# Optimization experiments

Hardware: AMD Instinct MI355X
Metric: run time of the kernel (lower is better)

Reference implementation:

```python
import jax, jax.numpy as jnp
import numpy as np
import math

EPS = 1e-5

def make_coords(H, W):
    # Faithful port of generate_coordinates (batch-independent; channels 8,9 stay zero).
    cy = H / 2.0 - 0.5
    cx = W / 2.0 - 0.5
    gx, gy = np.meshgrid(np.arange(H, dtype=np.float32), np.arange(W, dtype=np.float32), indexing='ij')
    two_pi = 2.0 * math.pi
    theta = np.arctan2(gy - cx, gx - cy) % two_pi
    theta = np.round(10000.0 * theta) / 10000.0
    coords = np.zeros((H, W, 18), dtype=np.float32)
    adds = [(1, 1), (1, 0), (1, -1), (0, 1), None, (0, -1), (-1, 1), (-1, 0), (-1, -1)]
    for k, add in enumerate(adds):
        if add is None:
            continue  # center tap offset left at zero (as in source)
        n = k if k < 4 else k - 1
        a = theta + n * (two_pi / 8.0)
        coords[:, :, 2 * k] = np.cos(a) + add[0]
        coords[:, :, 2 * k + 1] = np.sin(a) + add[1]
    return jnp.asarray(coords)

def bilinear_sample(x, py, px):
    # x: [B,C,H,W]; py/px: [H,W] sample coords; zero outside boundaries (torchvision semantics).
    H, W = x.shape[2], x.shape[3]
    y0f = jnp.floor(py); x0f = jnp.floor(px)
    wy1 = py - y0f; wy0 = 1.0 - wy1
    wx1 = px - x0f; wx0 = 1.0 - wx1
    def gather(yf, xf):
        valid = ((yf >= 0) & (yf < H) & (xf >= 0) & (xf < W)).astype(x.dtype)
        yi = jnp.clip(yf, 0, H - 1).astype(jnp.int32)
        xi = jnp.clip(xf, 0, W - 1).astype(jnp.int32)
        return x[:, :, yi, xi] * valid  # [B,C,H,W]
    return (gather(y0f, x0f) * (wy0 * wx0) + gather(y0f, x0f + 1) * (wy0 * wx1)
            + gather(y0f + 1, x0f) * (wy1 * wx0) + gather(y0f + 1, x0f + 1) * (wy1 * wx1))

def deform_conv(x, coords, weight, pad=1):
    # x: [B,Cin,H,W]; coords: [H,W,18] with (dy,dx) pairs per 3x3 tap; weight: [Cout,Cin,3,3]; no bias.
    B, C, H, W = x.shape
    ys = jnp.arange(H, dtype=x.dtype)[:, None]
    xs = jnp.arange(W, dtype=x.dtype)[None, :]
    out = jnp.zeros((B, weight.shape[0], H, W), x.dtype)
    for k in range(9):  # fixed 3x3 taps
        kh, kw = k // 3, k % 3
        py = ys - pad + kh + coords[..., 2 * k]
        px = xs - pad + kw + coords[..., 2 * k + 1]
        samp = bilinear_sample(x, py, px)
        out = out + jnp.einsum('bchw,oc->bohw', samp, weight[:, :, kh, kw])
    return out

def bn_relu(x, gamma, beta):
    # BatchNorm2d in training mode (batch statistics, biased variance) + ReLU.
    mu = x.mean(axis=(0, 2, 3), keepdims=True)
    var = ((x - mu) ** 2).mean(axis=(0, 2, 3), keepdims=True)
    xn = (x - mu) * jax.lax.rsqrt(var + EPS)
    return jax.nn.relu(xn * gamma[None, :, None, None] + beta[None, :, None, None])

def maxpool2(x):
    B, C, H, W = x.shape
    return x.reshape(B, C, H // 2, 2, W // 2, 2).max(axis=(3, 5))

def setup_inputs() -> dict:
    key = jax.random.key(0)
    ks = jax.random.split(key, 16)
    B = 1024
    def conv_w(k, co, ci):
        return jax.random.normal(k, (co, ci, 3, 3), jnp.float32) * (1.0 / np.sqrt(ci * 9))
    inp = {
        'x': jax.random.normal(ks[0], (B, 1, 32, 32), jnp.float32),
        'w11': conv_w(ks[1], 32, 1),  'g11': jnp.ones(32),  'b11': jnp.zeros(32),
        'w12': conv_w(ks[2], 32, 32), 'g12': jnp.ones(32),  'b12': jnp.zeros(32),
        'w21': conv_w(ks[3], 64, 32), 'g21': jnp.ones(64),  'b21': jnp.zeros(64),
        'w22': conv_w(ks[4], 64, 64), 'g22': jnp.ones(64),  'b22': jnp.zeros(64),
        'w31': conv_w(ks[5], 128, 64),  'g31': jnp.ones(128), 'b31': jnp.zeros(128),
        'w32': conv_w(ks[6], 128, 128), 'g32': jnp.ones(128), 'b32': jnp.zeros(128),
        'fcw': jax.random.normal(ks[7], (10, 128), jnp.float32) * (1.0 / np.sqrt(128)),
        'fcb': jnp.zeros(10),
        'c32': make_coords(32, 32),
        'c16': make_coords(16, 16),
        'c8': make_coords(8, 8),
    }
    return inp

def reference(x, w11, g11, b11, w12, g12, b12, w21, g21, b21, w22, g22, b22,
              w31, g31, b31, w32, g32, b32, fcw, fcb, c32, c16, c8):
    x = bn_relu(deform_conv(x, c32, w11), g11, b11)
    x = bn_relu(deform_conv(x, c32, w12), g12, b12)
    x = maxpool2(x)                      # [B,32,16,16]
    x = bn_relu(deform_conv(x, c16, w21), g21, b21)
    x = bn_relu(deform_conv(x, c16, w22), g22, b22)
    x = maxpool2(x)                      # [B,64,8,8]
    x = bn_relu(deform_conv(x, c8, w31), g31, b31)
    x = bn_relu(deform_conv(x, c8, w32), g32, b32)
    x = x.mean(axis=(2, 3))              # AvgPool2d(8) over full 8x8 -> [B,128]
    return x @ fcw.T + fcb               # [B,10]
```

## Files before the change

### kernel.cpp

```cpp
#include <hip/hip_runtime.h>
#include <math.h>


#define BATCH 1024
typedef unsigned short u16;
typedef unsigned int uint;
typedef __attribute__((ext_vector_type(8))) short short8;
typedef __attribute__((ext_vector_type(4))) float f32x4;
typedef __attribute__((ext_vector_type(2))) float f32x2;

__device__ __forceinline__ float b2f(u16 v) {
    return __uint_as_float(((uint)v) << 16);
}
__device__ __forceinline__ float4 b2f4(ushort4 v) {
    return make_float4(b2f(v.x), b2f(v.y), b2f(v.z), b2f(v.w));
}
__device__ __forceinline__ u16 f2b(float f) {
    uint u = __float_as_uint(f);
    return (u16)((u + 0x7FFFu + ((u >> 16) & 1u)) >> 16);
}
__device__ __forceinline__ float ldf(const void* p, long long i, int isbf) {
    return isbf ? b2f(((const u16*)p)[i]) : ((const float*)p)[i];
}
__device__ __forceinline__ f32x2 upk(uint u) {
    f32x2 r;
    r.x = __uint_as_float(u << 16);
    r.y = __uint_as_float(u & 0xFFFF0000u);
    return r;
}

struct Ptrs { const void* p[24]; int sz[24]; };

__global__ __launch_bounds__(256) void probe_dtype(Ptrs P, int* __restrict__ flags)
{
    int t = blockIdx.x;
    bool ones = (t == 2 || t == 5 || t == 8 || t == 11 || t == 14 || t == 17);
    bool inh  = (t == 3 || t == 6 || t == 9 || t == 12 || t == 15 || t == 18 || t == 20);
    if (inh) return;
    const u16* q = (const u16*)P.p[t];
    if (ones) {
        if (threadIdx.x == 0) {
            uint w0 = *(const uint*)q;
            flags[t] = (w0 == 0x3F803F80u) ? 1 : 0;
        }
        return;
    }
    int n = P.sz[t]; if (n > 4096) n = 4096;
    __shared__ int cnt;
    if (threadIdx.x == 0) cnt = 0;
    __syncthreads();
    int local = 0;
    for (int i = threadIdx.x; i < n; i += 256) {
        uint e = (q[i] >> 7) & 0xFFu;
        if (!(e == 0u || (e >= 100u && e <= 140u))) local++;
    }
    atomicAdd(&cnt, local);
    __syncthreads();
    if (threadIdx.x == 0) flags[t] = (cnt * 8 > n) ? 0 : 1;
}

__global__ void fixup_flags(int* __restrict__ flags)
{
    if (threadIdx.x == 0) {
        flags[3] = flags[2];  flags[6] = flags[5];  flags[9] = flags[8];
        flags[12] = flags[11]; flags[15] = flags[14]; flags[18] = flags[17];
        flags[20] = flags[19];
    }
}

__device__ void table_body(const void* coords, int H, int W,
                           int* tIdx, float* tW, int fcd, int i)
{
    int HW = H * W;
    if (i >= HW * 9) return;
    int p = i / 9, k = i % 9;
    int h = p / W, w = p % W;
    int kh = k / 3, kw = k % 3;
    float py = (float)(h - 1 + kh) + ldf(coords, p * 18 + 2 * k, fcd);
    float px = (float)(w - 1 + kw) + ldf(coords, p * 18 + 2 * k + 1, fcd);
    float y0f = floorf(py), x0f = floorf(px);
    float wy1 = py - y0f, wy0 = 1.0f - wy1;
    float wx1 = px - x0f, wx0 = 1.0f - wx1;
    int y0 = (int)y0f, x0 = (int)x0f;
#pragma unroll
    for (int j = 0; j < 4; ++j) {
        int dy = j >> 1, dx = j & 1;
        int yy = y0 + dy, xx = x0 + dx;
        bool valid = (yy >= 0) && (yy < H) && (xx >= 0) && (xx < W);
        int yc = min(max(yy, 0), H - 1);
        int xc = min(max(xx, 0), W - 1);
        tIdx[i * 4 + j] = yc * W + xc;
        tW[i * 4 + j] = valid ? (dy ? wy1 : wy0) * (dx ? wx1 : wx0) : 0.0f;
    }
}

__global__ __launch_bounds__(256) void build_tables(
    const void* c32, const void* c16, const void* c8,
    int* tI32, float* tW32, int* tI16, float* tW16, int* tI8, float* tW8,
    const int* __restrict__ flags)
{
    int b = blockIdx.x, t = threadIdx.x;
    if (b < 36)      table_body(c32, 32, 32, tI32, tW32, flags[21], b * 256 + t);
    else if (b < 45) table_body(c16, 16, 16, tI16, tW16, flags[22], (b - 36) * 256 + t);
    else             table_body(c8, 8, 8, tI8, tW8, flags[23], (b - 45) * 256 + t);
}

__global__ __launch_bounds__(256) void transpose_in(
    const void* __restrict__ x, u16* __restrict__ X0, const int* __restrict__ flags)
{
    int fx = flags[0];
    int p = blockIdx.x;
    int t = threadIdx.x;
    ushort4 v;
    v.x = f2b(ldf(x, (long long)(4 * t + 0) * 1024 + p, fx));
    v.y = f2b(ldf(x, (long long)(4 * t + 1) * 1024 + p, fx));
    v.z = f2b(ldf(x, (long long)(4 * t + 2) * 1024 + p, fx));
    v.w = f2b(ldf(x, (long long)(4 * t + 3) * 1024 + p, fx));
    ((ushort4*)(X0 + (size_t)p * BATCH))[t] = v;
}

__device__ void wb_body(const void* W, u16* Wb, int Cout, int Cin, int fw, int i)
{
    int c8 = i & 7;
    int r = i >> 3;
    int m = r % Cout;
    int r2 = r / Cout;
    int noct = Cin >> 3;
    int oc = r2 % noct;
    int k = r2 / noct;
    int c = oc * 8 + c8;
    Wb[i] = f2b(ldf(W, (long long)m * Cin * 9 + c * 9 + k, fw));
}

__global__ __launch_bounds__(256) void prep_all(
    const void* w11, const void* w12, const void* w21, const void* w22,
    const void* w31, const void* w32,
    float* w11p, u16* wb12, u16* wb21, u16* wb22, u16* wb31, u16* wb32,
    const int* __restrict__ flags)
{
    int i = blockIdx.x * 256 + threadIdx.x;
    if (i < 288) {
        int o = i / 9, k = i % 9;
        w11p[k * 32 + o] = ldf(w11, i, flags[1]);
    } else if (i < 9504)   wb_body(w12, wb12, 32, 32, flags[4], i - 288);
    else if (i < 27936)    wb_body(w21, wb21, 64, 32, flags[7], i - 9504);
    else if (i < 64800)    wb_body(w22, wb22, 64, 64, flags[10], i - 27936);
    else if (i < 138528)   wb_body(w31, wb31, 128, 64, flags[13], i - 64800);
    else if (i < 285984)   wb_body(w32, wb32, 128, 128, flags[16], i - 138528);
}

__global__ __launch_bounds__(256) void conv_l11(
    const u16* __restrict__ X0, const float* __restrict__ W2,
    u16* __restrict__ Y, const int* __restrict__ tIdx, const float* __restrict__ tW)
{
    const int id = blockIdx.x;
    const int p = id >> 1;
    const int oBase = (id & 1) * 16;
    const int b4 = threadIdx.x;
    const ushort4* Xu = (const ushort4*)X0;

    float4 acc[16];
#pragma unroll
    for (int o = 0; o < 16; ++o) acc[o] = make_float4(0.f, 0.f, 0.f, 0.f);

#pragma unroll
    for (int k = 0; k < 9; ++k) {
        float4 s = make_float4(0.f, 0.f, 0.f, 0.f);
#pragma unroll
        for (int j = 0; j < 4; ++j) {
            float wgt = tW[p * 36 + k * 4 + j];
            int pix = tIdx[p * 36 + k * 4 + j];
            float4 v = b2f4(Xu[pix * 256 + b4]);
            s.x = fmaf(wgt, v.x, s.x); s.y = fmaf(wgt, v.y, s.y);
            s.z = fmaf(wgt, v.z, s.z); s.w = fmaf(wgt, v.w, s.w);
        }
#pragma unroll
        for (int o = 0; o < 16; ++o) {
            float wv = W2[k * 32 + oBase + o];
            acc[o].x = fmaf(wv, s.x, acc[o].x); acc[o].y = fmaf(wv, s.y, acc[o].y);
            acc[o].z = fmaf(wv, s.z, acc[o].z); acc[o].w = fmaf(wv, s.w, acc[o].w);
        }
    }
#pragma unroll
    for (int bb = 0; bb < 4; ++bb) {
        u16 h[16];
#pragma unroll
        for (int o = 0; o < 16; ++o) h[o] = f2b((&acc[o].x)[bb]);
        uint4 pk;
        pk.x = (uint)h[0] | ((uint)h[1] << 16);
        pk.y = (uint)h[2] | ((uint)h[3] << 16);
        pk.z = (uint)h[4] | ((uint)h[5] << 16);
        pk.w = (uint)h[6] | ((uint)h[7] << 16);
        uint4 pk2;
        pk2.x = (uint)h[8] | ((uint)h[9] << 16);
        pk2.y = (uint)h[10] | ((uint)h[11] << 16);
        pk2.z = (uint)h[12] | ((uint)h[13] << 16);
        pk2.w = (uint)h[14] | ((uint)h[15] << 16);
        size_t base = ((size_t)p * 1024 + 4 * b4 + bb) * 32 + oBase;
        *(uint4*)(Y + base) = pk;
        *(uint4*)(Y + base + 8) = pk2;
    }
}

template<int MF, int NF, int BNORM>
__global__ __launch_bounds__(256) void conv_mfma(
    const u16* __restrict__ X, const u16* __restrict__ Wb,
    u16* __restrict__ Y,
    const int* __restrict__ tIdx, const float* __restrict__ tW,
    int Cin, int Cout, int HW, int pshift,
    const float* __restrict__ stats, const void* __restrict__ gamma,
    const void* __restrict__ beta, const int* __restrict__ flags,
    int gslot, int bslot, float invN)
{
    __shared__ float sSC[128], sSH[128];
    if (BNORM) {
        if (threadIdx.x < Cin) {
            int c = threadIdx.x;
            float mean = stats[2 * c] * invN;
            float var = stats[2 * c + 1] * invN - mean * mean;
            float sc = ldf(gamma, c, flags[gslot]) * rsqrtf(var + 1e-5f);
            sSC[c] = sc;
            sSH[c] = ldf(beta, c, flags[bslot]) - mean * sc;
        }
        __syncthreads();
    }

    const int tid = threadIdx.x;
    const int wid = tid >> 6;
    const int lane = tid & 63;
    const int quad = lane >> 4;
    const int l16 = lane & 15;

    const int pper = HW >> 3;
    const int xcd = blockIdx.x & 7;
    const int lid = blockIdx.x >> 3;
    const int p = xcd * pper + (lid & (pper - 1));
    const int yq = lid >> pshift;

    const int nb = yq * (4 * NF * 16);
    const int wn = wid * (NF * 16);

    const int noct = Cin >> 3;
    const size_t pixstride = (size_t)1024 * Cin;

    int roff[NF];
#pragma unroll
    for (int nf = 0; nf < NF; ++nf)
        roff[nf] = (nb + wn + nf * 16 + l16) * Cin + quad * 8;

    f32x4 acc[MF][NF];
#pragma unroll
    for (int mf = 0; mf < MF; ++mf)
#pragma unroll
        for (int nf = 0; nf < NF; ++nf)
            acc[mf][nf] = (f32x4){0.f, 0.f, 0.f, 0.f};

    const f32x2 zero2 = (f32x2){0.f, 0.f};
    const int nc = Cin >> 5;
    for (int cc = 0; cc < nc; ++cc) {
        const int coff = cc << 5;
        f32x2 sc2[4], sh2[4];
        if (BNORM) {
            int c0 = coff + quad * 8;
#pragma unroll
            for (int i = 0; i < 4; ++i) {
                sc2[i] = *(const f32x2*)(sSC + c0 + 2 * i);
                sh2[i] = *(const f32x2*)(sSH + c0 + 2 * i);
            }
        }
        for (int k = 0; k < 9; ++k) {
            int pix[4]; f32x2 ww[4];
#pragma unroll
            for (int j = 0; j < 4; ++j) {
                pix[j] = __builtin_amdgcn_readfirstlane(tIdx[p * 36 + k * 4 + j]);
                float w = __uint_as_float(__builtin_amdgcn_readfirstlane(
                    __float_as_uint(tW[p * 36 + k * 4 + j])));
                ww[j].x = w; ww[j].y = w;
            }
            const u16* xb0 = X + (size_t)pix[0] * pixstride;
            const u16* xb1 = X + (size_t)pix[1] * pixstride;
            const u16* xb2 = X + (size_t)pix[2] * pixstride;
            const u16* xb3 = X + (size_t)pix[3] * pixstride;

            short8 bf[NF];
#pragma unroll
            for (int nf = 0; nf < NF; ++nf) {
                int ro = roff[nf] + coff;
                uint4 v0 = *(const uint4*)(xb0 + ro);
                uint4 v1 = *(const uint4*)(xb1 + ro);
                uint4 v2 = *(const uint4*)(xb2 + ro);
                uint4 v3 = *(const uint4*)(xb3 + ro);
                const uint* a0 = &v0.x; const uint* a1 = &v1.x;
                const uint* a2 = &v2.x; const uint* a3 = &v3.x;
                union { short8 s; uint4 u; } cvt;
                uint o[4];
#pragma unroll
                for (int i = 0; i < 4; ++i) {
                    f32x2 t0 = upk(a0[i]), t1 = upk(a1[i]);
                    f32x2 t2 = upk(a2[i]), t3 = upk(a3[i]);
                    if (BNORM) {
                        t0 = __builtin_elementwise_max(t0 * sc2[i] + sh2[i], zero2);
                        t1 = __builtin_elementwise_max(t1 * sc2[i] + sh2[i], zero2);
                        t2 = __builtin_elementwise_max(t2 * sc2[i] + sh2[i], zero2);
                        t3 = __builtin_elementwise_max(t3 * sc2[i] + sh2[i], zero2);
                    }
                    f32x2 a = t0 * ww[0];
                    a = t1 * ww[1] + a;
                    a = t2 * ww[2] + a;
                    a = t3 * ww[3] + a;
                    o[i] = __builtin_amdgcn_perm(
                        __float_as_uint(a.y) + 0x8000u,
                        __float_as_uint(a.x) + 0x8000u, 0x07060302u);
                }
                cvt.u.x = o[0]; cvt.u.y = o[1]; cvt.u.z = o[2]; cvt.u.w = o[3];
                bf[nf] = cvt.s;
            }
            const u16* wk = Wb + ((size_t)(k * noct + (cc << 2) + quad) * Cout + l16) * 8;
#pragma unroll
            for (int mf = 0; mf < MF; ++mf) {
                const short8 af = *(const short8*)(wk + (size_t)mf * 16 * 8);
#pragma unroll
                for (int nf = 0; nf < NF; ++nf)
                    acc[mf][nf] = __builtin_amdgcn_mfma_f32_16x16x32_bf16(
                        af, bf[nf], acc[mf][nf], 0, 0, 0);
            }
        }
    }

#pragma unroll
    for (int mf = 0; mf < MF; ++mf) {
        int cout0 = mf * 16 + quad * 4;
#pragma unroll
        for (int nf = 0; nf < NF; ++nf) {
            int b = nb + wn + nf * 16 + l16;
            ushort4 pk;
            pk.x = f2b(acc[mf][nf][0]);
            pk.y = f2b(acc[mf][nf][1]);
            pk.z = f2b(acc[mf][nf][2]);
            pk.w = f2b(acc[mf][nf][3]);
            *(ushort4*)(Y + ((size_t)p * 1024 + b) * Cout + cout0) = pk;
        }
    }
}

__global__ __launch_bounds__(256) void bn_stats2(
    const u16* __restrict__ Y, float* __restrict__ stats, int Cin, long long NPB)
{
    const int stride = Cin >> 3;
    const int RPI = 256 / stride;
    const int t = threadIdx.x;
    const int cg = t % stride;
    const int r = t / stride;
    const int lane = t & 63;
    const int wid = t >> 6;

    float s[8], q[8];
#pragma unroll
    for (int j = 0; j < 8; ++j) { s[j] = 0.f; q[j] = 0.f; }

    for (long long row0 = (long long)blockIdx.x * RPI; row0 < NPB;
         row0 += (long long)gridDim.x * RPI) {
        long long row = row0 + r;
        if (row >= NPB) continue;
        uint4 v = *(const uint4*)(Y + row * Cin + cg * 8);
        uint ua[4] = {v.x, v.y, v.z, v.w};
#pragma unroll
        for (int jj = 0; jj < 4; ++jj) {
            float lo = __uint_as_float(ua[jj] << 16);
            float hi = __uint_as_float(ua[jj] & 0xFFFF0000u);
            s[2 * jj] += lo;     q[2 * jj] += lo * lo;
            s[2 * jj + 1] += hi; q[2 * jj + 1] += hi * hi;
        }
    }
    for (int off = 32; off >= stride; off >>= 1) {
#pragma unroll
        for (int j = 0; j < 8; ++j) {
            s[j] += __shfl_down(s[j], off);
            q[j] += __shfl_down(q[j], off);
        }
    }
    __shared__ float rs[4][128], rq[4][128];
    if (lane < stride) {
#pragma unroll
        for (int j = 0; j < 8; ++j) {
            rs[wid][lane * 8 + j] = s[j];
            rq[wid][lane * 8 + j] = q[j];
        }
    }
    __syncthreads();
    if (t < Cin) {
        float S = rs[0][t] + rs[1][t] + rs[2][t] + rs[3][t];
        float Q = rq[0][t] + rq[1][t] + rq[2][t] + rq[3][t];
        atomicAdd(&stats[2 * t], S);
        atomicAdd(&stats[2 * t + 1], Q);
    }
}

__global__ __launch_bounds__(256) void pool_bn(
    const u16* __restrict__ A, u16* __restrict__ P,
    const float* __restrict__ stats,
    const void* __restrict__ gamma, const void* __restrict__ beta,
    const int* __restrict__ flags, int gslot, int bslot,
    int H2, int W2, int C, float invN, long long total)
{
    __shared__ float sSC[128], sSH[128];
    if (threadIdx.x < C) {
        int c = threadIdx.x;
        float mean = stats[2 * c] * invN;
        float var = stats[2 * c + 1] * invN - mean * mean;
        float sc = ldf(gamma, c, flags[gslot]) * rsqrtf(var + 1e-5f);
        sSC[c] = sc;
        sSH[c] = ldf(beta, c, flags[bslot]) - mean * sc;
    }
    __syncthreads();
    long long i = (long long)blockIdx.x * 256 + threadIdx.x;
    if (i >= total) return;
    int cgn = C >> 3;
    int cg = (int)(i % cgn);
    long long row = i / cgn;
    int b = (int)(row & 1023);
    int p2 = (int)(row >> 10);
    int h2 = p2 / W2, w2 = p2 % W2;
    int W = 2 * W2;
    int p00 = (2 * h2) * W + 2 * w2;
    const u16* base = A + (size_t)cg * 8;
    uint4 va = *(const uint4*)(base + ((size_t)(p00)*1024 + b) * C);
    uint4 vb = *(const uint4*)(base + ((size_t)(p00 + 1) * 1024 + b) * C);
    uint4 vd = *(const uint4*)(base + ((size_t)(p00 + W) * 1024 + b) * C);
    uint4 ve = *(const uint4*)(base + ((size_t)(p00 + W + 1) * 1024 + b) * C);
    uint ra[4] = {va.x, va.y, va.z, va.w};
    uint rb[4] = {vb.x, vb.y, vb.z, vb.w};
    uint rd[4] = {vd.x, vd.y, vd.z, vd.w};
    uint re[4] = {ve.x, ve.y, ve.z, ve.w};
    uint ro[4];
#pragma unroll
    for (int j = 0; j < 4; ++j) {
        int c = cg * 8 + 2 * j;
        float lo = fmaxf(fmaxf(__uint_as_float(ra[j] << 16), __uint_as_float(rb[j] << 16)),
                         fmaxf(__uint_as_float(rd[j] << 16), __uint_as_float(re[j] << 16)));
        float hi = fmaxf(fmaxf(__uint_as_float(ra[j] & 0xFFFF0000u), __uint_as_float(rb[j] & 0xFFFF0000u)),
                         fmaxf(__uint_as_float(rd[j] & 0xFFFF0000u), __uint_as_float(re[j] & 0xFFFF0000u)));
        lo = fmaxf(fmaf(lo, sSC[c], sSH[c]), 0.f);
        hi = fmaxf(fmaf(hi, sSC[c + 1], sSH[c + 1]), 0.f);
        ro[j] = ((uint)f2b(hi) << 16) | (uint)f2b(lo);
    }
    uint4 m; m.x = ro[0]; m.y = ro[1]; m.z = ro[2]; m.w = ro[3];
    *(uint4*)(P + ((size_t)p2 * 1024 + b) * C + cg * 8) = m;
}

__global__ __launch_bounds__(256) void avg_bn(
    const u16* __restrict__ A, float* __restrict__ M,
    const float* __restrict__ stats,
    const void* __restrict__ gamma, const void* __restrict__ beta,
    const int* __restrict__ flags, int gslot, int bslot, float invN)
{
    __shared__ float sSC[128], sSH[128];
    if (threadIdx.x < 128) {
        int c = threadIdx.x;
        float mean = stats[2 * c] * invN;
        float var = stats[2 * c + 1] * invN - mean * mean;
        float sc = ldf(gamma, c, flags[gslot]) * rsqrtf(var + 1e-5f);
        sSC[c] = sc;
        sSH[c] = ldf(beta, c, flags[bslot]) - mean * sc;
    }
    __syncthreads();
    int i = blockIdx.x * 256 + threadIdx.x;
    int b = i >> 4, cg = i & 15;
    float s[8];
#pragma unroll
    for (int j = 0; j < 8; ++j) s[j] = 0.f;
    for (int p = 0; p < 64; ++p) {
        uint4 v = *(const uint4*)(A + ((size_t)p * 1024 + b) * 128 + cg * 8);
        uint ua[4] = {v.x, v.y, v.z, v.w};
#pragma unroll
        for (int jj = 0; jj < 4; ++jj) {
            int c = cg * 8 + 2 * jj;
            float lo = __uint_as_float(ua[jj] << 16);
            float hi = __uint_as_float(ua[jj] & 0xFFFF0000u);
            s[2 * jj] += fmaxf(fmaf(lo, sSC[c], sSH[c]), 0.f);
            s[2 * jj + 1] += fmaxf(fmaf(hi, sSC[c + 1], sSH[c + 1]), 0.f);
        }
    }
#pragma unroll
    for (int j = 0; j < 8; ++j) M[(size_t)b * 128 + cg * 8 + j] = s[j] * (1.0f / 64.0f);
}

__global__ __launch_bounds__(256) void fc_naive(
    const float* __restrict__ M, const void* __restrict__ fcw,
    const void* __restrict__ fcb, float* __restrict__ out, int total,
    const int* __restrict__ flags)
{
    int fw = flags[19], fb = flags[20];
    int i = blockIdx.x * 256 + threadIdx.x;
    if (i >= total) return;
    int o = i % 10, b = i / 10;
    float acc = ldf(fcb, o, fb);
    const float* Mb = M + (size_t)b * 128;
    for (int c = 0; c < 128; ++c) acc = fmaf(Mb[c], ldf(fcw, (size_t)o * 128 + c, fw), acc);
    out[i] = acc;
}

__global__ __launch_bounds__(256) void sentinel_k(float* out, int n, float v) {
    int i = blockIdx.x * 256 + threadIdx.x;
    if (i < n) out[i] = v;
}

extern "C" void kernel_launch(void* const* d_in, const int* in_sizes, int n_in,
                              void* d_out, int out_size, void* d_ws, size_t ws_size,
                              hipStream_t stream) {
    float* out = (float*)d_out;

    static const int exp_sizes[24] = {
        1024 * 1024,
        288, 32, 32,   9216, 32, 32,   18432, 64, 64,   36864, 64, 64,
        73728, 128, 128,   147456, 128, 128,
        1280, 10,   18432, 4608, 1152
    };
    float bad = 0.0f;
    if (n_in != 24) bad = 1000.0f;
    else {
        for (int i = 0; i < 24; ++i)
            if (in_sizes[i] != exp_sizes[i]) { bad = 2000.0f + 16.0f * i; break; }
    }
    if (bad != 0.0f) {
        sentinel_k<<<(out_size + 255) / 256, 256, 0, stream>>>(out, out_size, bad);
        return;
    }

    Ptrs P;
    for (int i = 0; i < 24; ++i) { P.p[i] = d_in[i]; P.sz[i] = in_sizes[i]; }

    char* wsb = (char*)d_ws;
    size_t off = 0;
    auto take = [&](size_t bytes) -> void* {
        void* pp = wsb + off;
        off += (bytes + 255) & ~(size_t)255;
        return pp;
    };
    int*   flags = (int*)  take(32 * 4);
    float* stats = (float*)take(6 * 256 * 4);
    int*   tI32  = (int*)  take(1024 * 36 * 4);
    float* tW32  = (float*)take(1024 * 36 * 4);
    int*   tI16  = (int*)  take(256 * 36 * 4);
    float* tW16  = (float*)take(256 * 36 * 4);
    int*   tI8   = (int*)  take(64 * 36 * 4);
    float* tW8   = (float*)take(64 * 36 * 4);
    float* w11p  = (float*)take(32 * 9 * 4);
    u16*   wb12  = (u16*)  take(32 * 32 * 9 * 2);
    u16*   wb21  = (u16*)  take(64 * 32 * 9 * 2);
    u16*   wb22  = (u16*)  take(64 * 64 * 9 * 2);
    u16*   wb31  = (u16*)  take(128 * 64 * 9 * 2);
    u16*   wb32  = (u16*)  take(128 * 128 * 9 * 2);
    u16*   X0    = (u16*)  take((size_t)1024 * BATCH * 2);
    float* M     = (float*)take((size_t)BATCH * 128 * 4);
    u16*   bufA  = (u16*)  take((size_t)32 * 1024 * BATCH * 2);
    u16*   bufB  = (u16*)  take((size_t)32 * 1024 * BATCH * 2);

    if (ws_size < off) {
        sentinel_k<<<(out_size + 255) / 256, 256, 0, stream>>>(out, out_size, 12345.0f);
        return;
    }

    probe_dtype<<<24, 256, 0, stream>>>(P, flags);
    fixup_flags<<<1, 64, 0, stream>>>(flags);
    hipMemsetAsync(stats, 0, 6 * 256 * 4, stream);
    build_tables<<<48, 256, 0, stream>>>(d_in[21], d_in[22], d_in[23],
                                         tI32, tW32, tI16, tW16, tI8, tW8, flags);
    transpose_in<<<1024, 256, 0, stream>>>(d_in[0], X0, flags);
    prep_all<<<1118, 256, 0, stream>>>(d_in[1], d_in[4], d_in[7], d_in[10], d_in[13], d_in[16],
                                       w11p, wb12, wb21, wb22, wb31, wb32, flags);

    float* st0 = stats + 0 * 256;
    float* st1 = stats + 1 * 256;
    float* st2 = stats + 2 * 256;
    float* st3 = stats + 3 * 256;
    float* st4 = stats + 4 * 256;
    float* st5 = stats + 5 * 256;

    conv_l11<<<2048, 256, 0, stream>>>(X0, w11p, bufA, tI32, tW32);
    bn_stats2<<<256, 256, 0, stream>>>(bufA, st0, 32, 1048576LL);
    conv_mfma<2, 2, 1><<<8192, 256, 0, stream>>>(bufA, wb12, bufB, tI32, tW32, 32, 32, 1024, 7,
                                                 st0, d_in[2], d_in[3], flags, 2, 3, 1.0f / 1048576.0f);
    bn_stats2<<<256, 256, 0, stream>>>(bufB, st1, 32, 1048576LL);
    pool_bn<<<4096, 256, 0, stream>>>(bufB, bufA, st1, d_in[5], d_in[6], flags, 5, 6,
                                      16, 16, 32, 1.0f / 1048576.0f, 1048576LL);
    conv_mfma<4, 2, 0><<<2048, 256, 0, stream>>>(bufA, wb21, bufB, tI16, tW16, 32, 64, 256, 5,
                                                 st0, d_in[2], d_in[3], flags, 2, 3, 0.f);
    bn_stats2<<<256, 256, 0, stream>>>(bufB, st2, 64, 262144LL);
    conv_mfma<4, 2, 1><<<2048, 256, 0, stream>>>(bufB, wb22, bufA, tI16, tW16, 64, 64, 256, 5,
                                                 st2, d_in[8], d_in[9], flags, 8, 9, 1.0f / 262144.0f);
    bn_stats2<<<256, 256, 0, stream>>>(bufA, st3, 64, 262144LL);
    pool_bn<<<2048, 256, 0, stream>>>(bufA, bufB, st3, d_in[11], d_in[12], flags, 11, 12,
                                      8, 8, 64, 1.0f / 262144.0f, 524288LL);
    conv_mfma<8, 1, 0><<<1024, 256, 0, stream>>>(bufB, wb31, bufA, tI8, tW8, 64, 128, 64, 3,
                                                 st0, d_in[2], d_in[3], flags, 2, 3, 0.f);
    bn_stats2<<<256, 256, 0, stream>>>(bufA, st4, 128, 65536LL);
    conv_mfma<8, 1, 1><<<1024, 256, 0, stream>>>(bufA, wb32, bufB, tI8, tW8, 128, 128, 64, 3,
                                                 st4, d_in[14], d_in[15], flags, 14, 15, 1.0f / 65536.0f);
    bn_stats2<<<256, 256, 0, stream>>>(bufB, st5, 128, 65536LL);
    avg_bn<<<64, 256, 0, stream>>>(bufB, M, st5, d_in[17], d_in[18], flags, 17, 18,
                                   1.0f / 65536.0f);
    fc_naive<<<40, 256, 0, stream>>>(M, d_in[19], d_in[20], out, 10240, flags);
}
```

Measured before the change: 871.8 us.

## Switch activation storage and MFMA from bf16 to fp16 with packed half math

Changes all intermediate activations and weights from bf16 to fp16, switches the MFMA instruction to the f16 variant, and performs the bilinear gather-combine and BN+ReLU in packed f16x2 arithmetic instead of unpacking to f32 pairs. This is meant to halve the ALU work of the sampling/normalization inner loop and remove the manual bf16 rounding/perm steps. A new bn_apply2 kernel is added, though its use is not shown. It risks overflow or precision loss given fp16's narrower range, especially for unnormalized conv outputs.

Measured after the change: 865.5 us. About the same (-0.7%).

```diff
diff --git a/kernel.cpp b/kernel.cpp
--- a/kernel.cpp
+++ b/kernel.cpp
@@ -5,28 +5,33 @@
 #define BATCH 1024
 typedef unsigned short u16;
 typedef unsigned int uint;
-typedef __attribute__((ext_vector_type(8))) short short8;
+typedef _Float16 f16;
+typedef __attribute__((ext_vector_type(2))) _Float16 f16x2;
+typedef __attribute__((ext_vector_type(8))) _Float16 f16x8;
 typedef __attribute__((ext_vector_type(4))) float f32x4;
-typedef __attribute__((ext_vector_type(2))) float f32x2;
 
 __device__ __forceinline__ float b2f(u16 v) {
     return __uint_as_float(((uint)v) << 16);
 }
-__device__ __forceinline__ float4 b2f4(ushort4 v) {
-    return make_float4(b2f(v.x), b2f(v.y), b2f(v.z), b2f(v.w));
-}
-__device__ __forceinline__ u16 f2b(float f) {
-    uint u = __float_as_uint(f);
-    return (u16)((u + 0x7FFFu + ((u >> 16) & 1u)) >> 16);
-}
 __device__ __forceinline__ float ldf(const void* p, long long i, int isbf) {
     return isbf ? b2f(((const u16*)p)[i]) : ((const float*)p)[i];
 }
-__device__ __forceinline__ f32x2 upk(uint u) {
-    f32x2 r;
-    r.x = __uint_as_float(u << 16);
-    r.y = __uint_as_float(u & 0xFFFF0000u);
-    return r;
+__device__ __forceinline__ f16x2 u2h2(uint u) {
+    union { uint u; f16x2 h; } c; c.u = u; return c.h;
+}
+__device__ __forceinline__ uint h22u(f16x2 h) {
+    union { uint u; f16x2 h; } c; c.h = h; return c.u;
+}
+__device__ __forceinline__ float h2f(u16 v) {
+    union { u16 u; f16 h; } c; c.u = v; return (float)c.h;
+}
+__device__ __forceinline__ u16 f2h(float f) {
+    union { u16 u; f16 h; } c; c.h = (f16)f; return c.u;
+}
+__device__ __forceinline__ f16x2 pkh(float a, float b) {
+    union { decltype(__builtin_amdgcn_cvt_pkrtz(0.f, 0.f)) v; f16x2 h; } c;
+    c.v = __builtin_amdgcn_cvt_pkrtz(a, b);
+    return c.h;
 }
 
 struct Ptrs { const void* p[24]; int sz[24]; };
@@ -112,10 +117,10 @@
     int p = blockIdx.x;
     int t = threadIdx.x;
     ushort4 v;
-    v.x = f2b(ldf(x, (long long)(4 * t + 0) * 1024 + p, fx));
-    v.y = f2b(ldf(x, (long long)(4 * t + 1) * 1024 + p, fx));
-    v.z = f2b(ldf(x, (long long)(4 * t + 2) * 1024 + p, fx));
-    v.w = f2b(ldf(x, (long long)(4 * t + 3) * 1024 + p, fx));
+    v.x = f2h(ldf(x, (long long)(4 * t + 0) * 1024 + p, fx));
+    v.y = f2h(ldf(x, (long long)(4 * t + 1) * 1024 + p, fx));
+    v.z = f2h(ldf(x, (long long)(4 * t + 2) * 1024 + p, fx));
+    v.w = f2h(ldf(x, (long long)(4 * t + 3) * 1024 + p, fx));
     ((ushort4*)(X0 + (size_t)p * BATCH))[t] = v;
 }
 
@@ -129,7 +134,7 @@
     int oc = r2 % noct;
     int k = r2 / noct;
     int c = oc * 8 + c8;
-    Wb[i] = f2b(ldf(W, (long long)m * Cin * 9 + c * 9 + k, fw));
+    Wb[i] = f2h(ldf(W, (long long)m * Cin * 9 + c * 9 + k, fw));
 }
 
 __global__ __launch_bounds__(256) void prep_all(
@@ -170,9 +175,9 @@
         for (int j = 0; j < 4; ++j) {
             float wgt = tW[p * 36 + k * 4 + j];
             int pix = tIdx[p * 36 + k * 4 + j];
-            float4 v = b2f4(Xu[pix * 256 + b4]);
-            s.x = fmaf(wgt, v.x, s.x); s.y = fmaf(wgt, v.y, s.y);
-            s.z = fmaf(wgt, v.z, s.z); s.w = fmaf(wgt, v.w, s.w);
+            ushort4 vv = Xu[pix * 256 + b4];
+            s.x = fmaf(wgt, h2f(vv.x), s.x); s.y = fmaf(wgt, h2f(vv.y), s.y);
+            s.z = fmaf(wgt, h2f(vv.z), s.z); s.w = fmaf(wgt, h2f(vv.w), s.w);
         }
 #pragma unroll
         for (int o = 0; o < 16; ++o) {
@@ -185,7 +190,7 @@
     for (int bb = 0; bb < 4; ++bb) {
         u16 h[16];
 #pragma unroll
-        for (int o = 0; o < 16; ++o) h[o] = f2b((&acc[o].x)[bb]);
+        for (int o = 0; o < 16; ++o) h[o] = f2h((&acc[o].x)[bb]);
         uint4 pk;
         pk.x = (uint)h[0] | ((uint)h[1] << 16);
         pk.y = (uint)h[2] | ((uint)h[3] << 16);
@@ -255,34 +260,34 @@
         for (int nf = 0; nf < NF; ++nf)
             acc[mf][nf] = (f32x4){0.f, 0.f, 0.f, 0.f};
 
-    const f32x2 zero2 = (f32x2){0.f, 0.f};
+    const f16x2 zeroh = (f16x2){(f16)0, (f16)0};
     const int nc = Cin >> 5;
     for (int cc = 0; cc < nc; ++cc) {
         const int coff = cc << 5;
-        f32x2 sc2[4], sh2[4];
+        f16x2 sc2[4], sh2[4];
         if (BNORM) {
             int c0 = coff + quad * 8;
 #pragma unroll
             for (int i = 0; i < 4; ++i) {
-                sc2[i] = *(const f32x2*)(sSC + c0 + 2 * i);
-                sh2[i] = *(const f32x2*)(sSH + c0 + 2 * i);
+                sc2[i] = pkh(sSC[c0 + 2 * i], sSC[c0 + 2 * i + 1]);
+                sh2[i] = pkh(sSH[c0 + 2 * i], sSH[c0 + 2 * i + 1]);
             }
         }
         for (int k = 0; k < 9; ++k) {
-            int pix[4]; f32x2 ww[4];
+            int pix[4]; f16x2 wwh[4];
 #pragma unroll
             for (int j = 0; j < 4; ++j) {
                 pix[j] = __builtin_amdgcn_readfirstlane(tIdx[p * 36 + k * 4 + j]);
                 float w = __uint_as_float(__builtin_amdgcn_readfirstlane(
                     __float_as_uint(tW[p * 36 + k * 4 + j])));
-                ww[j].x = w; ww[j].y = w;
+                wwh[j] = pkh(w, w);
             }
             const u16* xb0 = X + (size_t)pix[0] * pixstride;
             const u16* xb1 = X + (size_t)pix[1] * pixstride;
             const u16* xb2 = X + (size_t)pix[2] * pixstride;
             const u16* xb3 = X + (size_t)pix[3] * pixstride;
 
-            short8 bf[NF];
+            f16x8 bf[NF];
 #pragma unroll
             for (int nf = 0; nf < NF; ++nf) {
                 int ro = roff[nf] + coff;
@@ -292,36 +297,34 @@
                 uint4 v3 = *(const uint4*)(xb3 + ro);
                 const uint* a0 = &v0.x; const uint* a1 = &v1.x;
                 const uint* a2 = &v2.x; const uint* a3 = &v3.x;
-                union { short8 s; uint4 u; } cvt;
+                union { f16x8 h; uint4 u; } cvt;
                 uint o[4];
 #pragma unroll
                 for (int i = 0; i < 4; ++i) {
-                    f32x2 t0 = upk(a0[i]), t1 = upk(a1[i]);
-                    f32x2 t2 = upk(a2[i]), t3 = upk(a3[i]);
+                    f16x2 t0 = u2h2(a0[i]), t1 = u2h2(a1[i]);
+                    f16x2 t2 = u2h2(a2[i]), t3 = u2h2(a3[i]);
                     if (BNORM) {
-                        t0 = __builtin_elementwise_max(t0 * sc2[i] + sh2[i], zero2);
-                        t1 = __builtin_elementwise_max(t1 * sc2[i] + sh2[i], zero2);
-                        t2 = __builtin_elementwise_max(t2 * sc2[i] + sh2[i], zero2);
-                        t3 = __builtin_elementwise_max(t3 * sc2[i] + sh2[i], zero2);
+                        t0 = __builtin_elementwise_max(t0 * sc2[i] + sh2[i], zeroh);
+                        t1 = __builtin_elementwise_max(t1 * sc2[i] + sh2[i], zeroh);
+                        t2 = __builtin_elementwise_max(t2 * sc2[i] + sh2[i], zeroh);
+                        t3 = __builtin_elementwise_max(t3 * sc2[i] + sh2[i], zeroh);
                     }
-                    f32x2 a = t0 * ww[0];
-                    a = t1 * ww[1] + a;
-                    a = t2 * ww[2] + a;
-                    a = t3 * ww[3] + a;
-                    o[i] = __builtin_amdgcn_perm(
-                        __float_as_uint(a.y) + 0x8000u,
-                        __float_as_uint(a.x) + 0x8000u, 0x07060302u);
+                    f16x2 a = t0 * wwh[0];
+                    a = t1 * wwh[1] + a;
+                    a = t2 * wwh[2] + a;
+                    a = t3 * wwh[3] + a;
+                    o[i] = h22u(a);
                 }
                 cvt.u.x = o[0]; cvt.u.y = o[1]; cvt.u.z = o[2]; cvt.u.w = o[3];
-                bf[nf] = cvt.s;
+                bf[nf] = cvt.h;
             }
             const u16* wk = Wb + ((size_t)(k * noct + (cc << 2) + quad) * Cout + l16) * 8;
 #pragma unroll
             for (int mf = 0; mf < MF; ++mf) {
-                const short8 af = *(const short8*)(wk + (size_t)mf * 16 * 8);
+                const f16x8 af = *(const f16x8*)(wk + (size_t)mf * 16 * 8);
 #pragma unroll
                 for (int nf = 0; nf < NF; ++nf)
-                    acc[mf][nf] = __builtin_amdgcn_mfma_f32_16x16x32_bf16(
+                    acc[mf][nf] = __builtin_amdgcn_mfma_f32_16x16x32_f16(
                         af, bf[nf], acc[mf][nf], 0, 0, 0);
             }
         }
@@ -333,12 +336,10 @@
 #pragma unroll
         for (int nf = 0; nf < NF; ++nf) {
             int b = nb + wn + nf * 16 + l16;
-            ushort4 pk;
-            pk.x = f2b(acc[mf][nf][0]);
-            pk.y = f2b(acc[mf][nf][1]);
-            pk.z = f2b(acc[mf][nf][2]);
-            pk.w = f2b(acc[mf][nf][3]);
-            *(ushort4*)(Y + ((size_t)p * 1024 + b) * Cout + cout0) = pk;
+            uint2 pk;
+            pk.x = h22u(pkh(acc[mf][nf][0], acc[mf][nf][1]));
+            pk.y = h22u(pkh(acc[mf][nf][2], acc[mf][nf][3]));
+            *(uint2*)(Y + ((size_t)p * 1024 + b) * Cout + cout0) = pk;
         }
     }
 }
@@ -366,8 +367,8 @@
         uint ua[4] = {v.x, v.y, v.z, v.w};
 #pragma unroll
         for (int jj = 0; jj < 4; ++jj) {
-            float lo = __uint_as_float(ua[jj] << 16);
-            float hi = __uint_as_float(ua[jj] & 0xFFFF0000u);
+            f16x2 h = u2h2(ua[jj]);
+            float lo = (float)h.x, hi = (float)h.y;
             s[2 * jj] += lo;     q[2 * jj] += lo * lo;
             s[2 * jj + 1] += hi; q[2 * jj + 1] += hi * hi;
         }
@@ -393,6 +394,43 @@
         float Q = rq[0][t] + rq[1][t] + rq[2][t] + rq[3][t];
         atomicAdd(&stats[2 * t], S);
         atomicAdd(&stats[2 * t + 1], Q);
+    }
+}
+
+__global__ __launch_bounds__(256) void bn_apply2(
+    u16* __restrict__ Y, const float* __restrict__ stats,
+    const void* __restrict__ gamma, const void* __restrict__ beta,
+    int Cin, float invN, long long total8,
+    const int* __restrict__ flags, int gslot, int bslot)
+{
+    __shared__ float sSC[128], sSH[128];
+    int fg = flags[gslot], fb = flags[bslot];
+    if (threadIdx.x < Cin) {
+        int c = threadIdx.x;
+        float mean = stats[2 * c] * invN;
+        float var = stats[2 * c + 1] * invN - mean * mean;
+        float sc = ldf(gamma, c, fg) * rsqrtf(var + 1e-5f);
+        sSC[c] = sc;
+        sSH[c] = ldf(beta, c, fb) - mean * sc;
+    }
+    __syncthreads();
+    const int stride = Cin >> 3;
+    for (long long i = (long long)blockIdx.x * 256 + threadIdx.x; i < total8;
+         i += (long long)gridDim.x * 256) {
+        int cg = (int)(i % stride);
+        uint4* ptr = (uint4*)(Y + i * 8);
+        uint4 v = *ptr;
+        uint ua[4] = {v.x, v.y, v.z, v.w};
+#pragma unroll
+        for (int jj = 0; jj < 4; ++jj) {
+            int c = cg * 8 + 2 * jj;
+            f16x2 h = u2h2(ua[jj]);
+            float lo = fmaxf(fmaf((float)h.x, sSC[c], sSH[c]), 0.f);
+            float hi = fmaxf(fmaf((float)h.y, sSC[c + 1], sSH[c + 1]), 0.f);
+            ua[jj] = h22u(pkh(lo, hi));
+        }
+        v.x = ua[0]; v.y = ua[1]; v.z = ua[2]; v.w = ua[3];
+        *ptr = v;
     }
 }
 
@@ -436,13 +474,12 @@
 #pragma unroll
     for (int j = 0; j < 4; ++j) {
         int c = cg * 8 + 2 * j;
-        float lo = fmaxf(fmaxf(__uint_as_float(ra[j] << 16), __uint_as_float(rb[j] << 16)),
-                         fmaxf(__uint_as_float(rd[j] << 16), __uint_as_float(re[j] << 16)));
-        float hi = fmaxf(fmaxf(__uint_as_float(ra[j] & 0xFFFF0000u), __uint_as_float(rb[j] & 0xFFFF0000u)),
-                         fmaxf(__uint_as_float(rd[j] & 0xFFFF0000u), __uint_as_float(re[j] & 0xFFFF0000u)));
-        lo = fmaxf(fmaf(lo, sSC[c], sSH[c]), 0.f);
-        hi = fmaxf(fmaf(hi, sSC[c + 1], sSH[c + 1]), 0.f);
-        ro[j] = ((uint)f2b(hi) << 16) | (uint)f2b(lo);
+        f16x2 ha = u2h2(ra[j]), hb = u2h2(rb[j]), hd = u2h2(rd[j]), he = u2h2(re[j]);
+        f16x2 hm = __builtin_elementwise_max(
+            __builtin_elementwise_max(ha, hb), __builtin_elementwise_max(hd, he));
+        float lo = fmaxf(fmaf((float)hm.x, sSC[c], sSH[c]), 0.f);
+        float hi = fmaxf(fmaf((float)hm.y, sSC[c + 1], sSH[c + 1]), 0.f);
+        ro[j] = h22u(pkh(lo, hi));
     }
     uint4 m; m.x = ro[0]; m.y = ro[1]; m.z = ro[2]; m.w = ro[3];
     *(uint4*)(P + ((size_t)p2 * 1024 + b) * C + cg * 8) = m;
@@ -475,10 +512,9 @@
 #pragma unroll
         for (int jj = 0; jj < 4; ++jj) {
             int c = cg * 8 + 2 * jj;
-            float lo = __uint_as_float(ua[jj] << 16);
-            float hi = __uint_as_float(ua[jj] & 0xFFFF0000u);
-            s[2 * jj] += fmaxf(fmaf(lo, sSC[c], sSH[c]), 0.f);
-            s[2 * jj + 1] += fmaxf(fmaf(hi, sSC[c + 1], sSH[c + 1]), 0.f);
+            f16x2 h = u2h2(ua[jj]);
+            s[2 * jj] += fmaxf(fmaf((float)h.x, sSC[c], sSH[c]), 0.f);
+            s[2 * jj + 1] += fmaxf(fmaf((float)h.y, sSC[c + 1], sSH[c + 1]), 0.f);
         }
     }
 #pragma unroll
```
